# Kernel optimization log

Hardware: AMD Instinct MI355X
Metric: run time of the kernel (lower is better)

Reference implementation:

```python
import jax, jax.numpy as jnp
import numpy as np

B, T_HIST, D, H, STEPS = 2048, 15, 64, 128, 20
MAX_STEPS = 48           # max adaptive steps per unit time interval
DT0, RTOL, ATOL = 0.1, 1e-3, 1e-6
SAFETY, FMIN, FMAX = 0.9, 0.2, 10.0

# Tsit5 (Tsitouras 2011) tableau
A21 = 0.161
A31, A32 = -0.008480655492356989, 0.335480655492357
A41, A42, A43 = 2.8971530571054935, -6.359448489975075, 4.3622954328695815
A51, A52, A53, A54 = 5.325864828439257, -11.748883564062828, 7.4955393428898365, -0.09249506636175525
A61, A62, A63, A64, A65 = 5.86145544294642, -12.92096931784711, 8.159367898576159, -0.071584973281401, -0.028269050394068383
B1, B2, B3, B4, B5, B6 = 0.09646076681806523, 0.01, 0.4798896504144996, 1.379008574103742, -3.290069515436081, 2.324710524099774
E1, E2, E3, E4, E5, E6, E7 = (-0.00178001105222577714, -0.0008164344596567469, 0.007880878010261995,
                              -0.1447110071732629, 0.5823571654525552, -0.45808210592918697, 0.015151515151515152)


def _mlp(y, W1, b1, W2, b2, W3, b3):
    h = jax.nn.softplus(y @ W1.T + b1)
    h = jax.nn.softplus(h @ W2.T + b2)
    return h @ W3.T + b3


def _solve(y0, W1, b1, W2, b2, W3, b3, steps):
    f = lambda y: _mlp(y, W1, b1, W2, b2, W3, b3)  # batched vector field [B,D]->[B,D]
    Bn = y0.shape[0]

    def segment(carry, t1):
        y, dt = carry
        t = jnp.full((Bn,), t1 - 1.0, y0.dtype)
        done = jnp.zeros((Bn,), bool)

        def body(state, _):
            t, y, dt, done = state
            dt_c = jnp.minimum(dt, t1 - t)          # clip to segment end
            h = dt_c[:, None]
            k1 = f(y)
            k2 = f(y + h * (A21 * k1))
            k3 = f(y + h * (A31 * k1 + A32 * k2))
            k4 = f(y + h * (A41 * k1 + A42 * k2 + A43 * k3))
            k5 = f(y + h * (A51 * k1 + A52 * k2 + A53 * k3 + A54 * k4))
            k6 = f(y + h * (A61 * k1 + A62 * k2 + A63 * k3 + A64 * k4 + A65 * k5))
            y5 = y + h * (B1 * k1 + B2 * k2 + B3 * k3 + B4 * k4 + B5 * k5 + B6 * k6)
            k7 = f(y5)
            err = h * (E1 * k1 + E2 * k2 + E3 * k3 + E4 * k4 + E5 * k5 + E6 * k6 + E7 * k7)
            scale = ATOL + RTOL * jnp.maximum(jnp.abs(y), jnp.abs(y5))
            err_norm = jnp.sqrt(jnp.mean((err / scale) ** 2, axis=-1))  # [B]
            accept = (err_norm <= 1.0) & (~done)
            factor = jnp.clip(SAFETY * jnp.maximum(err_norm, 1e-10) ** (-0.2), FMIN, FMAX)
            t_new = jnp.where(accept, t + dt_c, t)
            y_new = jnp.where(accept[:, None], y5, y)
            dt_new = jnp.where(done, dt, dt_c * factor)
            done_new = done | (t_new >= t1 - 1e-8)
            return (t_new, y_new, dt_new, done_new), None

        (t, y, dt, done), _ = jax.lax.scan(jax.checkpoint(body), (t, y, dt, done), None, length=MAX_STEPS)
        return (y, dt), y

    ts1 = jnp.arange(1, steps + 1, dtype=y0.dtype)
    dt0 = jnp.full((Bn,), DT0, y0.dtype)
    (_, _), ys = jax.lax.scan(segment, (y0, dt0), ts1)  # ys: [steps, B, D]
    return jnp.transpose(ys, (1, 0, 2))                  # [B, steps, D]


def setup_inputs() -> dict:
    key = jax.random.key(0)
    ks = jax.random.split(key, 7)
    history = jax.random.normal(ks[0], (B, T_HIST, D), jnp.float32)
    # small-scale init keeps the vector field mild so adaptive steps converge
    W1 = jax.random.normal(ks[1], (H, D), jnp.float32) * (0.5 / np.sqrt(D))
    b1 = jax.random.normal(ks[2], (H,), jnp.float32) * 0.05
    W2 = jax.random.normal(ks[3], (H, H), jnp.float32) * (0.5 / np.sqrt(H))
    b2 = jax.random.normal(ks[4], (H,), jnp.float32) * 0.05
    W3 = jax.random.normal(ks[5], (D, H), jnp.float32) * (0.1 / np.sqrt(H))
    b3 = jax.random.normal(ks[6], (D,), jnp.float32) * 0.05
    return {"history": history, "W1": W1, "b1": b1, "W2": W2, "b2": b2, "W3": W3, "b3": b3, "steps": STEPS}


def reference(history, W1, b1, W2, b2, W3, b3, steps):
    y0 = history[:, -1]  # NeuralODE uses only the last history state
    return _solve(y0, W1, b1, W2, b2, W3, b3, steps)
```

## Files before the change

kernel.cpp:

```cpp
#include <hip/hip_runtime.h>
#include <math.h>

#define NB    2048
#define NSEG  20
#define MAXIT 48
#define CH    544
#define BLKS  136

typedef __attribute__((ext_vector_type(8))) short bf8_t;
typedef __attribute__((ext_vector_type(4))) float f32x4;

#define cA21 ((float)0.161)
#define cA31 ((float)-0.008480655492356989)
#define cA32 ((float)0.335480655492357)
#define cA41 ((float)2.8971530571054935)
#define cA42 ((float)-6.359448489975075)
#define cA43 ((float)4.3622954328695815)
#define cA51 ((float)5.325864828439257)
#define cA52 ((float)-11.748883564062828)
#define cA53 ((float)7.4955393428898365)
#define cA54 ((float)-0.09249506636175525)
#define cA61 ((float)5.86145544294642)
#define cA62 ((float)-12.92096931784711)
#define cA63 ((float)8.159367898576159)
#define cA64 ((float)-0.071584973281401)
#define cA65 ((float)-0.028269050394068383)
#define cB1  ((float)0.09646076681806523)
#define cB2  ((float)0.01)
#define cB3  ((float)0.4798896504144996)
#define cB4  ((float)1.379008574103742)
#define cB5  ((float)-3.290069515436081)
#define cB6  ((float)2.324710524099774)
#define cE1  ((float)-0.001780011052225777)
#define cE2  ((float)-0.0008164344596567469)
#define cE3  ((float)0.007880878010261995)
#define cE4  ((float)-0.1447110071732629)
#define cE5  ((float)0.5823571654525552)
#define cE6  ((float)-0.45808210592918697)
#define cE7  ((float)0.015151515151515152)

__device__ __forceinline__ void split2(float x, short &hi, short &lo) {
    unsigned u = __float_as_uint(x);
    hi = (short)(u >> 16);
    float r = x - __uint_as_float(u & 0xFFFF0000u);
    lo = (short)(__float_as_uint(r) >> 16);
}

__device__ __forceinline__ float softplus_f(float x) {
    float t = exp2f(-fabsf(x) * 1.442695040888963f);
    return fmaxf(x, 0.0f) + log2f(1.0f + t) * 0.6931471805599453f;
}

__device__ __forceinline__ unsigned pk(short a, short b) {
    return ((unsigned)(unsigned short)a) | (((unsigned)(unsigned short)b) << 16);
}

__device__ __forceinline__ float fold8(float x) {
    int r = __builtin_amdgcn_update_dpp(__float_as_int(x), __float_as_int(x),
                                        0x128, 0xF, 0xF, false);
    return x + __int_as_float(r);
}

__global__ __launch_bounds__(512)
void ode_kernel(const float* __restrict__ history,
                const float* __restrict__ W1, const float* __restrict__ b1,
                const float* __restrict__ W2, const float* __restrict__ b2,
                const float* __restrict__ W3, const float* __restrict__ b3,
                float* __restrict__ out)
{
    __shared__ alignas(16) short argB[2 * CH];
    __shared__ alignas(16) short h1B[4 * CH];
    __shared__ alignas(16) short h2B[4 * CH];
    __shared__ alignas(16) float kcur[8 * 68];
    __shared__ int doneF[8];

    const int tid  = threadIdx.x;
    const int wave = tid >> 6, lane = tid & 63;
    const int quad = lane >> 4, col = lane & 15;
    const int jb   = 16 * wave + 4 * quad;

    bf8_t A1h[2], A1l[2], A2h[4], A2l[4], A3h[4], A3l[4];
#pragma unroll
    for (int c = 0; c < 2; ++c) {
        const float* p = W1 + (size_t)(16 * wave + col) * 64 + 32 * c + 8 * quad;
        bf8_t h, l;
#pragma unroll
        for (int j = 0; j < 8; ++j) { short hs, ls; split2(p[j], hs, ls); h[j] = hs; l[j] = ls; }
        A1h[c] = h; A1l[c] = l;
    }
#pragma unroll
    for (int c = 0; c < 4; ++c) {
        const float* p = W2 + (size_t)(16 * wave + col) * 128 + 32 * c + 8 * quad;
        bf8_t h, l;
#pragma unroll
        for (int j = 0; j < 8; ++j) { short hs, ls; split2(p[j], hs, ls); h[j] = hs; l[j] = ls; }
        A2h[c] = h; A2l[c] = l;
    }
    f32x4 b3f = {0.f, 0.f, 0.f, 0.f};
    if (wave < 4) {
#pragma unroll
        for (int c = 0; c < 4; ++c) {
            const float* p = W3 + (size_t)(16 * wave + col) * 128 + 32 * c + 8 * quad;
            bf8_t h, l;
#pragma unroll
            for (int j = 0; j < 8; ++j) { short hs, ls; split2(p[j], hs, ls); h[j] = hs; l[j] = ls; }
            A3h[c] = h; A3l[c] = l;
        }
        b3f = *(const f32x4*)(b3 + jb);
    } else {
        bf8_t z = {0, 0, 0, 0, 0, 0, 0, 0};
#pragma unroll
        for (int c = 0; c < 4; ++c) { A3h[c] = z; A3l[c] = z; }
    }
    const f32x4 b1f = *(const f32x4*)(b1 + jb);
    const f32x4 b2f = *(const f32x4*)(b2 + jb);

    const int aidx = (lane >> 5) * CH + ((lane >> 3) & 3) * BLKS + wave * 8 + (lane & 7);
    const int elem = blockIdx.x * 8 + wave;

    const int esel  = col >> 3;
    const int eelem = col & 7;
    const int j0    = 16 * wave + 4 * quad + 2 * esel;
    const int epidx = (j0 >> 5) * CH + ((j0 >> 3) & 3) * BLKS + eelem * 8 + (j0 & 7);

    const int boff = quad * BLKS + col * 8;

    auto gemm = [&](const bf8_t* Ah, const bf8_t* Al, const short* Bc, int nch) -> f32x4 {
        f32x4 a0 = {0.f, 0.f, 0.f, 0.f}, a1 = a0;
#pragma unroll
        for (int c = 0; c < nch; ++c) {
            bf8_t b = *(const bf8_t*)(Bc + c * CH + boff);
            a0 = __builtin_amdgcn_mfma_f32_16x16x32_bf16(Ah[c], b, a0, 0, 0, 0);
            a1 = __builtin_amdgcn_mfma_f32_16x16x32_bf16(Al[c], b, a1, 0, 0, 0);
        }
        f32x4 s;
#pragma unroll
        for (int r = 0; r < 4; ++r) s[r] = a0[r] + a1[r];
        return s;
    };

    auto epi = [&](f32x4 s, f32x4 bias, short* Bn) {
        float t0 = fold8(s[0]) + bias[0];
        float t1 = fold8(s[1]) + bias[1];
        float t2 = fold8(s[2]) + bias[2];
        float t3 = fold8(s[3]) + bias[3];
        float x0 = esel ? t2 : t0;
        float x1 = esel ? t3 : t1;
        float p0 = softplus_f(x0), p1 = softplus_f(x1);
        short h0, l0, h1, l1;
        split2(p0, h0, l0);
        split2(p1, h1, l1);
        *(unsigned*)(Bn + epidx)      = pk(h0, h1);
        *(unsigned*)(Bn + epidx + 64) = pk(l0, l1);
    };

    auto eval = [&]() {
        __syncthreads();
        f32x4 s1 = gemm(A1h, A1l, argB, 2);
        epi(s1, b1f, h1B);
        __syncthreads();
        f32x4 s2 = gemm(A2h, A2l, h1B, 4);
        epi(s2, b2f, h2B);
        __syncthreads();
        if (wave < 4) {
            f32x4 s3 = gemm(A3h, A3l, h2B, 4);
            f32x4 kv;
#pragma unroll
            for (int r = 0; r < 4; ++r) kv[r] = fold8(s3[r]) + b3f[r];
            if (col < 8) *(f32x4*)(kcur + col * 68 + jb) = kv;
        }
        __syncthreads();
    };

    float y  = history[((size_t)elem * 15 + 14) * 64 + lane];
    float dt = 0.1f;
    float k1, k2, k3, k4, k5, k6;

    {
        short hi, lo; split2(y, hi, lo);
        argB[aidx] = hi; argB[aidx + 64] = lo;
        eval();
        k1 = kcur[wave * 68 + lane];
    }

#pragma unroll 1
    for (int seg = 1; seg <= NSEG; ++seg) {
        const float t1 = (float)seg;
        float t = t1 - 1.0f;
        bool done = false;

#pragma unroll 1
        for (int it = 0; it < MAXIT; ++it) {
            const float dt_c = fminf(dt, t1 - t);
            const float h = dt_c;
            float y5v = 0.f, k7v = 0.f;

#pragma unroll 1
            for (int st = 2; st <= 7; ++st) {
                float sum;
                switch (st) {
                    case 2: sum = cA21 * k1; break;
                    case 3: sum = fmaf(cA31, k1, cA32 * k2); break;
                    case 4: sum = fmaf(cA41, k1, fmaf(cA42, k2, cA43 * k3)); break;
                    case 5: sum = fmaf(cA51, k1, fmaf(cA52, k2, fmaf(cA53, k3, cA54 * k4))); break;
                    case 6: sum = fmaf(cA61, k1, fmaf(cA62, k2, fmaf(cA63, k3, fmaf(cA64, k4, cA65 * k5)))); break;
                    default: sum = fmaf(cB1, k1, fmaf(cB2, k2, fmaf(cB3, k3, fmaf(cB4, k4, fmaf(cB5, k5, cB6 * k6))))); break;
                }
                float arg = fmaf(h, sum, y);
                if (st == 7) y5v = arg;
                short hi, lo; split2(arg, hi, lo);
                argB[aidx] = hi; argB[aidx + 64] = lo;
                eval();
                float kv = kcur[wave * 68 + lane];
                switch (st) {
                    case 2: k2 = kv; break;
                    case 3: k3 = kv; break;
                    case 4: k4 = kv; break;
                    case 5: k5 = kv; break;
                    case 6: k6 = kv; break;
                    default: k7v = kv; break;
                }
            }

            float esum = fmaf(cE1, k1, fmaf(cE2, k2, fmaf(cE3, k3,
                         fmaf(cE4, k4, fmaf(cE5, k5, fmaf(cE6, k6, cE7 * k7v))))));
            float err = h * esum;
            float sc = fmaf(1e-3f, fmaxf(fabsf(y), fabsf(y5v)), 1e-6f);
            float r = err / sc;
            float rr = r * r;
#pragma unroll
            for (int off = 32; off > 0; off >>= 1) rr += __shfl_xor(rr, off, 64);
            float en = sqrtf(rr * (1.0f / 64.0f));

            bool accept = (en <= 1.0f) && !done;
            float fac = 0.9f * exp2f(-0.2f * log2f(fmaxf(en, 1e-10f)));
            fac = fminf(fmaxf(fac, 0.2f), 10.0f);

            if (accept) { t += dt_c; y = y5v; k1 = k7v; }
            if (!done) dt = dt_c * fac;
            done = done || (t >= t1 - 1e-8f);

            if (lane == 0) doneF[wave] = done ? 1 : 0;
            __syncthreads();
            bool all = true;
#pragma unroll
            for (int e2 = 0; e2 < 8; ++e2) all = all && (doneF[e2] != 0);
            if (all) break;
        }

        out[((size_t)elem * NSEG + (seg - 1)) * 64 + lane] = y;
    }
}

extern "C" void kernel_launch(void* const* d_in, const int* in_sizes, int n_in,
                              void* d_out, int out_size, void* d_ws, size_t ws_size,
                              hipStream_t stream) {
    const float* history = (const float*)d_in[0];
    const float* W1 = (const float*)d_in[1];
    const float* b1 = (const float*)d_in[2];
    const float* W2 = (const float*)d_in[3];
    const float* b2 = (const float*)d_in[4];
    const float* W3 = (const float*)d_in[5];
    const float* b3 = (const float*)d_in[6];
    float* out = (float*)d_out;

    ode_kernel<<<dim3(NB / 8), dim3(512), 0, stream>>>(history, W1, b1, W2, b2, W3, b3, out);
}
```

Before: 283.4 us.

## Keep ODE state in MFMA output layout to drop kcur LDS roundtrip

The solver state (y, k1..k7) now lives in the lanes that produce the layer-3 MFMA outputs. Each of waves 0-3 holds two dimensions for each of the 8 batch elements, replacing one-element-per-wave ownership. This removes the kcur shared-memory write/read and the trailing barrier in every MLP evaluation. The error-norm reduction becomes a cross-wave LDS partial sum with one barrier, and the all-done check uses a wave vote. In exchange, waves 4-7 sit idle during the stage arithmetic, and the layout indexing is more intricate.

```diff
diff --git a/kernel.cpp b/kernel.cpp
--- a/kernel.cpp
+++ b/kernel.cpp
@@ -71,8 +71,7 @@
     __shared__ alignas(16) short argB[2 * CH];
     __shared__ alignas(16) short h1B[4 * CH];
     __shared__ alignas(16) short h2B[4 * CH];
-    __shared__ alignas(16) float kcur[8 * 68];
-    __shared__ int doneF[8];
+    __shared__ float rrP[32];
 
     const int tid  = threadIdx.x;
     const int wave = tid >> 6, lane = tid & 63;
@@ -96,7 +95,12 @@
         for (int j = 0; j < 8; ++j) { short hs, ls; split2(p[j], hs, ls); h[j] = hs; l[j] = ls; }
         A2h[c] = h; A2l[c] = l;
     }
-    f32x4 b3f = {0.f, 0.f, 0.f, 0.f};
+    const int esel = col >> 3;
+    const int e    = col & 7;
+    const int d0   = 16 * wave + 4 * quad + 2 * esel;
+    const size_t elemIdx = (size_t)(blockIdx.x * 8 + e);
+
+    float b3v0 = 0.f, b3v1 = 0.f;
     if (wave < 4) {
 #pragma unroll
         for (int c = 0; c < 4; ++c) {
@@ -106,7 +110,7 @@
             for (int j = 0; j < 8; ++j) { short hs, ls; split2(p[j], hs, ls); h[j] = hs; l[j] = ls; }
             A3h[c] = h; A3l[c] = l;
         }
-        b3f = *(const f32x4*)(b3 + jb);
+        b3v0 = b3[d0]; b3v1 = b3[d0 + 1];
     } else {
         bf8_t z = {0, 0, 0, 0, 0, 0, 0, 0};
 #pragma unroll
@@ -115,13 +119,10 @@
     const f32x4 b1f = *(const f32x4*)(b1 + jb);
     const f32x4 b2f = *(const f32x4*)(b2 + jb);
 
-    const int aidx = (lane >> 5) * CH + ((lane >> 3) & 3) * BLKS + wave * 8 + (lane & 7);
-    const int elem = blockIdx.x * 8 + wave;
-
-    const int esel  = col >> 3;
-    const int eelem = col & 7;
+    const int ai = (d0 >> 5) * CH + ((d0 >> 3) & 3) * BLKS + e * 8 + (d0 & 7);
+
     const int j0    = 16 * wave + 4 * quad + 2 * esel;
-    const int epidx = (j0 >> 5) * CH + ((j0 >> 3) & 3) * BLKS + eelem * 8 + (j0 & 7);
+    const int epidx = (j0 >> 5) * CH + ((j0 >> 3) & 3) * BLKS + e * 8 + (j0 & 7);
 
     const int boff = quad * BLKS + col * 8;
 
@@ -154,7 +155,7 @@
         *(unsigned*)(Bn + epidx + 64) = pk(l0, l1);
     };
 
-    auto eval = [&]() {
+    auto eval = [&](float &kv0, float &kv1) {
         __syncthreads();
         f32x4 s1 = gemm(A1h, A1l, argB, 2);
         epi(s1, b1f, h1B);
@@ -164,24 +165,28 @@
         __syncthreads();
         if (wave < 4) {
             f32x4 s3 = gemm(A3h, A3l, h2B, 4);
-            f32x4 kv;
-#pragma unroll
-            for (int r = 0; r < 4; ++r) kv[r] = fold8(s3[r]) + b3f[r];
-            if (col < 8) *(f32x4*)(kcur + col * 68 + jb) = kv;
-        }
-        __syncthreads();
+            float f0 = fold8(s3[0]);
+            float f1 = fold8(s3[1]);
+            float f2 = fold8(s3[2]);
+            float f3 = fold8(s3[3]);
+            kv0 = (esel ? f2 : f0) + b3v0;
+            kv1 = (esel ? f3 : f1) + b3v1;
+        }
     };
 
-    float y  = history[((size_t)elem * 15 + 14) * 64 + lane];
+    float y0 = 0.f, y1 = 0.f;
     float dt = 0.1f;
-    float k1, k2, k3, k4, k5, k6;
-
-    {
-        short hi, lo; split2(y, hi, lo);
-        argB[aidx] = hi; argB[aidx + 64] = lo;
-        eval();
-        k1 = kcur[wave * 68 + lane];
-    }
+    float k1a = 0.f, k1b = 0.f, k2a, k2b, k3a, k3b, k4a, k4b, k5a, k5b, k6a, k6b;
+
+    if (wave < 4) {
+        float2 yy = *(const float2*)(history + (elemIdx * 15 + 14) * 64 + d0);
+        y0 = yy.x; y1 = yy.y;
+        short h0, l0, h1, l1;
+        split2(y0, h0, l0); split2(y1, h1, l1);
+        *(unsigned*)(argB + ai)      = pk(h0, h1);
+        *(unsigned*)(argB + ai + 64) = pk(l0, l1);
+    }
+    eval(k1a, k1b);
 
 #pragma unroll 1
     for (int seg = 1; seg <= NSEG; ++seg) {
@@ -193,62 +198,83 @@
         for (int it = 0; it < MAXIT; ++it) {
             const float dt_c = fminf(dt, t1 - t);
             const float h = dt_c;
-            float y5v = 0.f, k7v = 0.f;
+            float y50 = 0.f, y51 = 0.f, k7a = 0.f, k7b = 0.f;
 
 #pragma unroll 1
             for (int st = 2; st <= 7; ++st) {
-                float sum;
-                switch (st) {
-                    case 2: sum = cA21 * k1; break;
-                    case 3: sum = fmaf(cA31, k1, cA32 * k2); break;
-                    case 4: sum = fmaf(cA41, k1, fmaf(cA42, k2, cA43 * k3)); break;
-                    case 5: sum = fmaf(cA51, k1, fmaf(cA52, k2, fmaf(cA53, k3, cA54 * k4))); break;
-                    case 6: sum = fmaf(cA61, k1, fmaf(cA62, k2, fmaf(cA63, k3, fmaf(cA64, k4, cA65 * k5)))); break;
-                    default: sum = fmaf(cB1, k1, fmaf(cB2, k2, fmaf(cB3, k3, fmaf(cB4, k4, fmaf(cB5, k5, cB6 * k6))))); break;
+                if (wave < 4) {
+                    float sum0, sum1;
+                    switch (st) {
+                        case 2: sum0 = cA21 * k1a;
+                                sum1 = cA21 * k1b; break;
+                        case 3: sum0 = fmaf(cA31, k1a, cA32 * k2a);
+                                sum1 = fmaf(cA31, k1b, cA32 * k2b); break;
+                        case 4: sum0 = fmaf(cA41, k1a, fmaf(cA42, k2a, cA43 * k3a));
+                                sum1 = fmaf(cA41, k1b, fmaf(cA42, k2b, cA43 * k3b)); break;
+                        case 5: sum0 = fmaf(cA51, k1a, fmaf(cA52, k2a, fmaf(cA53, k3a, cA54 * k4a)));
+                                sum1 = fmaf(cA51, k1b, fmaf(cA52, k2b, fmaf(cA53, k3b, cA54 * k4b))); break;
+                        case 6: sum0 = fmaf(cA61, k1a, fmaf(cA62, k2a, fmaf(cA63, k3a, fmaf(cA64, k4a, cA65 * k5a))));
+                                sum1 = fmaf(cA61, k1b, fmaf(cA62, k2b, fmaf(cA63, k3b, fmaf(cA64, k4b, cA65 * k5b)))); break;
+                        default: sum0 = fmaf(cB1, k1a, fmaf(cB2, k2a, fmaf(cB3, k3a, fmaf(cB4, k4a, fmaf(cB5, k5a, cB6 * k6a)))));
+                                 sum1 = fmaf(cB1, k1b, fmaf(cB2, k2b, fmaf(cB3, k3b, fmaf(cB4, k4b, fmaf(cB5, k5b, cB6 * k6b))))); break;
+                    }
+                    float arg0 = fmaf(h, sum0, y0);
+                    float arg1 = fmaf(h, sum1, y1);
+                    if (st == 7) { y50 = arg0; y51 = arg1; }
+                    short h0, l0, h1, l1;
+                    split2(arg0, h0, l0); split2(arg1, h1, l1);
+                    *(unsigned*)(argB + ai)      = pk(h0, h1);
+                    *(unsigned*)(argB + ai + 64) = pk(l0, l1);
                 }
-                float arg = fmaf(h, sum, y);
-                if (st == 7) y5v = arg;
-                short hi, lo; split2(arg, hi, lo);
-                argB[aidx] = hi; argB[aidx + 64] = lo;
-                eval();
-                float kv = kcur[wave * 68 + lane];
-                switch (st) {
-                    case 2: k2 = kv; break;
-                    case 3: k3 = kv; break;
-                    case 4: k4 = kv; break;
-                    case 5: k5 = kv; break;
-                    case 6: k6 = kv; break;
-                    default: k7v = kv; break;
+                float kv0 = 0.f, kv1 = 0.f;
+                eval(kv0, kv1);
+                if (wave < 4) {
+                    switch (st) {
+                        case 2: k2a = kv0; k2b = kv1; break;
+                        case 3: k3a = kv0; k3b = kv1; break;
+                        case 4: k4a = kv0; k4b = kv1; break;
+                        case 5: k5a = kv0; k5b = kv1; break;
+                        case 6: k6a = kv0; k6b = kv1; break;
+                        default: k7a = kv0; k7b = kv1; break;
+                    }
                 }
             }
 
-            float esum = fmaf(cE1, k1, fmaf(cE2, k2, fmaf(cE3, k3,
-                         fmaf(cE4, k4, fmaf(cE5, k5, fmaf(cE6, k6, cE7 * k7v))))));
-            float err = h * esum;
-            float sc = fmaf(1e-3f, fmaxf(fabsf(y), fabsf(y5v)), 1e-6f);
-            float r = err / sc;
-            float rr = r * r;
-#pragma unroll
-            for (int off = 32; off > 0; off >>= 1) rr += __shfl_xor(rr, off, 64);
-            float en = sqrtf(rr * (1.0f / 64.0f));
+            float rr2 = 0.f;
+            if (wave < 4) {
+                float es0 = fmaf(cE1, k1a, fmaf(cE2, k2a, fmaf(cE3, k3a,
+                            fmaf(cE4, k4a, fmaf(cE5, k5a, fmaf(cE6, k6a, cE7 * k7a))))));
+                float es1 = fmaf(cE1, k1b, fmaf(cE2, k2b, fmaf(cE3, k3b,
+                            fmaf(cE4, k4b, fmaf(cE5, k5b, fmaf(cE6, k6b, cE7 * k7b))))));
+                float err0 = h * es0, err1 = h * es1;
+                float sc0 = fmaf(1e-3f, fmaxf(fabsf(y0), fabsf(y50)), 1e-6f);
+                float sc1 = fmaf(1e-3f, fmaxf(fabsf(y1), fabsf(y51)), 1e-6f);
+                float r0 = err0 / sc0, r1 = err1 / sc1;
+                rr2 = fmaf(r0, r0, r1 * r1);
+            }
+            rr2 += __shfl_xor(rr2, 16, 64);
+            rr2 += __shfl_xor(rr2, 32, 64);
+            rr2 = fold8(rr2);
+            if (wave < 4 && lane < 8) rrP[wave * 8 + lane] = rr2;
+            __syncthreads();
+            float rs = ((rrP[e] + rrP[8 + e]) + rrP[16 + e]) + rrP[24 + e];
+            float en = sqrtf(rs * (1.0f / 64.0f));
 
             bool accept = (en <= 1.0f) && !done;
             float fac = 0.9f * exp2f(-0.2f * log2f(fmaxf(en, 1e-10f)));
             fac = fminf(fmaxf(fac, 0.2f), 10.0f);
 
-            if (accept) { t += dt_c; y = y5v; k1 = k7v; }
+            if (wave < 4 && accept) { y0 = y50; y1 = y51; k1a = k7a; k1b = k7b; }
+            if (accept) t += dt_c;
             if (!done) dt = dt_c * fac;
             done = done || (t >= t1 - 1e-8f);
-
-            if (lane == 0) doneF[wave] = done ? 1 : 0;
-            __syncthreads();
-            bool all = true;
-#pragma unroll
-            for (int e2 = 0; e2 < 8; ++e2) all = all && (doneF[e2] != 0);
-            if (all) break;
-        }
-
-        out[((size_t)elem * NSEG + (seg - 1)) * 64 + lane] = y;
+            if (__all(done)) break;
+        }
+
+        if (wave < 4) {
+            float2 yy; yy.x = y0; yy.y = y1;
+            *(float2*)(out + (elemIdx * NSEG + (seg - 1)) * 64 + d0) = yy;
+        }
     }
 }
 
```

New measurement: 278.7 us (median of 2 runs). No clear change (-1.7%).
